# Kernel optimization log

Measured on AMD Instinct MI355X. Metric: run time of the kernel, lower is better.

Reference implementation:

```python
import jax, jax.numpy as jnp
import numpy as np
from jax import lax

N, C, L = 64, 64, 8192

def setup_inputs() -> dict:
    key = jax.random.key(0)
    k1, k2, k3 = jax.random.split(key, 3)
    observes = jax.random.normal(k1, (N, C, L), dtype=jnp.float32)
    transitions = jax.random.normal(k2, (C, C), dtype=jnp.float32) * 0.1
    target = jax.random.randint(k3, (N, L), 0, C, dtype=jnp.int64)
    return {"observes": observes, "transitions": transitions, "target": target}

def reference(observes, transitions, target):
    # Batched linear-chain CRF negative log-likelihood, averaged over batch.
    # observes: [N, C, L] emission scores; transitions: [C, C]; target: [N, L] int labels.
    em = jnp.transpose(observes, (0, 2, 1))  # [N, L, C]
    # Score of the gold path: emissions at gold labels + transitions between consecutive labels.
    gold_em = jnp.take_along_axis(em, target[..., None], axis=2)[..., 0].sum(axis=1)  # [N]
    gold_tr = transitions[target[:, :-1], target[:, 1:]].sum(axis=1)                  # [N]
    gold_score = gold_em + gold_tr
    # Forward algorithm (log-sum-exp DP over sequence length), batched over N.
    def step(alpha, e_t):
        # alpha: [N, C] log-scores ending in each state; e_t: [N, C]
        new_alpha = jax.nn.logsumexp(alpha[:, :, None] + transitions[None, :, :], axis=1) + e_t
        return new_alpha, None
    alpha0 = em[:, 0]                                  # [N, C]
    rest = jnp.moveaxis(em[:, 1:], 1, 0)               # [L-1, N, C] for scan
    alpha_T, _ = lax.scan(step, alpha0, rest)
    log_Z = jax.nn.logsumexp(alpha_T, axis=1)          # [N]
    nll = log_Z - gold_score                           # per-sample CRF loss
    return nll.sum() / nll.shape[0]
```

## Files before the change

### kernel.cpp

```cpp
#include <hip/hip_runtime.h>

#define NB 64
#define CS 64
#define LL 8192

#ifndef __has_builtin
#define __has_builtin(x) 0
#endif

__device__ __forceinline__ float uif(unsigned int u) { return __uint_as_float(u); }
__device__ __forceinline__ unsigned int fiu(float f) { return __float_as_uint(f); }

#define FMAC_DPP(ACC, Q, EV, R)                                                 \
  asm volatile("v_fmac_f32_dpp %0, %1, %2 row_ror:" #R                          \
               " row_mask:0xf bank_mask:0xf"                                    \
               : "+v"(ACC) : "v"(Q), "v"(EV))

#define ROW4(R)                                                                 \
  FMAC_DPP(acc0, qr0, Em[0][R], R);                                             \
  FMAC_DPP(acc1, qr1, Em[1][R], R);                                             \
  FMAC_DPP(acc2, qr2, Em[2][R], R);                                             \
  FMAC_DPP(acc3, qr3, Em[3][R], R)

__global__ __launch_bounds__(64, 1)
void crf_scan(const float* __restrict__ obs, const float* __restrict__ trans,
              float* __restrict__ out) {
  const int n = blockIdx.x;
  const int j = threadIdx.x;

  int w = __builtin_amdgcn_update_dpp(0, j, 0x121 , 0xf, 0xf, true);
  const int dsel = __builtin_amdgcn_readlane(w, 1);

  float Em[4][16];
#pragma unroll
  for (int g = 0; g < 4; ++g) {
#pragma unroll
    for (int r = 0; r < 16; ++r) {
      int irm = (j - r) & 15;
      int irp = (j + r) & 15;
      int ir = (dsel == 0) ? irm : irp;
      Em[g][r] = __expf(trans[(16 * g + ir) * CS + j]);
    }
  }

  const float* __restrict__ row = obs + ((size_t)n * CS + j) * (size_t)LL;
  float4 a0 = *(const float4*)(row);
  float4 a1 = *(const float4*)(row + 4);

  float q = __expf(a0.x);
  int carry = 0;

#pragma unroll 1
  for (int c = 0; c < LL / 8; ++c) {
    const int cn = (c + 1 < LL / 8) ? c + 1 : (LL / 8 - 1);
    float4 b0 = *(const float4*)(row + 8 * cn);
    float4 b1 = *(const float4*)(row + 8 * cn + 4);

    float ee[8];
    ee[0] = __expf(a0.x); ee[1] = __expf(a0.y);
    ee[2] = __expf(a0.z); ee[3] = __expf(a0.w);
    ee[4] = __expf(a1.x); ee[5] = __expf(a1.y);
    ee[6] = __expf(a1.z); ee[7] = __expf(a1.w);

#pragma unroll
    for (int k = 0; k < 8; ++k) {
      if (c == 0 && k == 0) continue;

#if __has_builtin(__builtin_amdgcn_permlane16_swap) && \
    __has_builtin(__builtin_amdgcn_permlane32_swap)
      unsigned qb = fiu(q);
      auto h = __builtin_amdgcn_permlane16_swap(qb, qb, false, false);
      auto A = __builtin_amdgcn_permlane32_swap(h[0], h[0], false, false);
      auto B = __builtin_amdgcn_permlane32_swap(h[1], h[1], false, false);
      float qr0 = uif(A[0]), qr2 = uif(A[1]);
      float qr1 = uif(B[0]), qr3 = uif(B[1]);
#else
      float qr0 = __shfl(q,  0 + (j & 15), 64);
      float qr1 = __shfl(q, 16 + (j & 15), 64);
      float qr2 = __shfl(q, 32 + (j & 15), 64);
      float qr3 = __shfl(q, 48 + (j & 15), 64);
#endif

      float acc0 = qr0 * Em[0][0];
      float acc1 = qr1 * Em[1][0];
      float acc2 = qr2 * Em[2][0];
      float acc3 = qr3 * Em[3][0];
      asm volatile("s_nop 1" :::);
      ROW4(1);  ROW4(2);  ROW4(3);  ROW4(4);  ROW4(5);
      ROW4(6);  ROW4(7);  ROW4(8);  ROW4(9);  ROW4(10);
      ROW4(11); ROW4(12); ROW4(13); ROW4(14); ROW4(15);
      float s = (acc0 + acc1) + (acc2 + acc3);
      q = s * ee[k];

      if ((k & 3) == 3) {
        unsigned q0 = (unsigned)__builtin_amdgcn_readfirstlane((int)fiu(q));
        int e = (int)((q0 >> 23) & 0xffu) - 126;
        q = ldexpf(q, -e);
        carry += e;
      }
    }
    a0 = b0; a1 = b1;
  }

  float s = q;
#pragma unroll
  for (int off = 32; off > 0; off >>= 1) s += __shfl_xor(s, off, 64);
  if (j == 0) {
    float logZ = (float)carry * 0.6931471805599453f + __logf(s);
    atomicAdd(out, logZ * (1.0f / NB));
  }
}

__global__ __launch_bounds__(256)
void crf_gold(const float* __restrict__ obs, const float* __restrict__ trans,
              const int* __restrict__ tgt, float* __restrict__ out) {
  const int n = blockIdx.x;
  const int tid = threadIdx.x;
  const int* __restrict__ trow = tgt + (size_t)n * LL;
  float acc = 0.f;
  for (int t = tid; t < LL; t += 256) {
    int s = trow[t];
    acc += obs[((size_t)n * CS + s) * (size_t)LL + t];
    if (t + 1 < LL) acc += trans[s * CS + trow[t + 1]];
  }
#pragma unroll
  for (int off = 32; off > 0; off >>= 1) acc += __shfl_xor(acc, off, 64);
  __shared__ float red[4];
  if ((tid & 63) == 0) red[tid >> 6] = acc;
  __syncthreads();
  if (tid == 0) {
    float tot = red[0] + red[1] + red[2] + red[3];
    atomicAdd(out, -tot * (1.0f / NB));
  }
}

extern "C" void kernel_launch(void* const* d_in, const int* in_sizes, int n_in,
                              void* d_out, int out_size, void* d_ws, size_t ws_size,
                              hipStream_t stream) {
  const float* obs   = (const float*)d_in[0];
  const float* trans = (const float*)d_in[1];
  const int*   tgt   = (const int*)d_in[2];
  float* out = (float*)d_out;

  hipMemsetAsync(out, 0, sizeof(float), stream);
  crf_gold<<<NB, 256, 0, stream>>>(obs, trans, tgt, out);
  crf_scan<<<NB, 64, 0, stream>>>(obs, trans, out);
}
```

Measured before the change: 1.664 ms.

## Fuse gold-score and forward-scan kernels into one launch

Merges the gold-path kernel and the forward-scan kernel into a single launch of 2*NB blocks. The first NB blocks run the scan on one wavefront and the rest compute the gold score, so both run concurrently instead of back to back. It also replaces ldexpf renormalisation with a direct exponent-bit subtraction, and turns the transition and emission arrays into named scalars so they stay in registers. Each scan block now reserves 256 threads while only 64 do work, and the bit-subtraction renormalisation does not handle denormal or zero values.

```diff
diff --git a/kernel.cpp b/kernel.cpp
--- a/kernel.cpp
+++ b/kernel.cpp
@@ -4,44 +4,48 @@
 #define CS 64
 #define LL 8192
 
-#ifndef __has_builtin
-#define __has_builtin(x) 0
-#endif
-
 __device__ __forceinline__ float uif(unsigned int u) { return __uint_as_float(u); }
 __device__ __forceinline__ unsigned int fiu(float f) { return __float_as_uint(f); }
 
-#define FMAC_DPP(ACC, Q, EV, R)                                                 \
+#define E_(G, R) Em_##G##_##R
+
+#define DECL_E16(G)                                                             \
+  float E_(G, 0), E_(G, 1), E_(G, 2), E_(G, 3), E_(G, 4), E_(G, 5), E_(G, 6),   \
+      E_(G, 7), E_(G, 8), E_(G, 9), E_(G, 10), E_(G, 11), E_(G, 12),            \
+      E_(G, 13), E_(G, 14), E_(G, 15)
+
+#define INIT_E(G, R)                                                            \
+  E_(G, R) = __expf(trans[(16 * G +                                             \
+                           ((dsel == 0) ? ((j - R) & 15) : ((j + R) & 15))) *   \
+                              CS +                                              \
+                          j])
+
+#define INIT_E16(G)                                                             \
+  INIT_E(G, 0);  INIT_E(G, 1);  INIT_E(G, 2);  INIT_E(G, 3);                    \
+  INIT_E(G, 4);  INIT_E(G, 5);  INIT_E(G, 6);  INIT_E(G, 7);                    \
+  INIT_E(G, 8);  INIT_E(G, 9);  INIT_E(G, 10); INIT_E(G, 11);                   \
+  INIT_E(G, 12); INIT_E(G, 13); INIT_E(G, 14); INIT_E(G, 15)
+
+#define FMAC_DPP(ACC, Q, G, R)                                                  \
   asm volatile("v_fmac_f32_dpp %0, %1, %2 row_ror:" #R                          \
                " row_mask:0xf bank_mask:0xf"                                    \
-               : "+v"(ACC) : "v"(Q), "v"(EV))
+               : "+v"(ACC) : "v"(Q), "v"(E_(G, R)))
 
 #define ROW4(R)                                                                 \
-  FMAC_DPP(acc0, qr0, Em[0][R], R);                                             \
-  FMAC_DPP(acc1, qr1, Em[1][R], R);                                             \
-  FMAC_DPP(acc2, qr2, Em[2][R], R);                                             \
-  FMAC_DPP(acc3, qr3, Em[3][R], R)
+  FMAC_DPP(acc0, qr0, 0, R);                                                    \
+  FMAC_DPP(acc1, qr1, 1, R);                                                    \
+  FMAC_DPP(acc2, qr2, 2, R);                                                    \
+  FMAC_DPP(acc3, qr3, 3, R)
 
-__global__ __launch_bounds__(64, 1)
-void crf_scan(const float* __restrict__ obs, const float* __restrict__ trans,
-              float* __restrict__ out) {
-  const int n = blockIdx.x;
-  const int j = threadIdx.x;
-
+__device__ __forceinline__ void crf_scan_block(const float* __restrict__ obs,
+                                               const float* __restrict__ trans,
+                                               float* __restrict__ out,
+                                               int n, int j) {
   int w = __builtin_amdgcn_update_dpp(0, j, 0x121 , 0xf, 0xf, true);
   const int dsel = __builtin_amdgcn_readlane(w, 1);
 
-  float Em[4][16];
-#pragma unroll
-  for (int g = 0; g < 4; ++g) {
-#pragma unroll
-    for (int r = 0; r < 16; ++r) {
-      int irm = (j - r) & 15;
-      int irp = (j + r) & 15;
-      int ir = (dsel == 0) ? irm : irp;
-      Em[g][r] = __expf(trans[(16 * g + ir) * CS + j]);
-    }
-  }
+  DECL_E16(0); DECL_E16(1); DECL_E16(2); DECL_E16(3);
+  INIT_E16(0); INIT_E16(1); INIT_E16(2); INIT_E16(3);
 
   const float* __restrict__ row = obs + ((size_t)n * CS + j) * (size_t)LL;
   float4 a0 = *(const float4*)(row);
@@ -56,47 +60,39 @@
     float4 b0 = *(const float4*)(row + 8 * cn);
     float4 b1 = *(const float4*)(row + 8 * cn + 4);
 
-    float ee[8];
-    ee[0] = __expf(a0.x); ee[1] = __expf(a0.y);
-    ee[2] = __expf(a0.z); ee[3] = __expf(a0.w);
-    ee[4] = __expf(a1.x); ee[5] = __expf(a1.y);
-    ee[6] = __expf(a1.z); ee[7] = __expf(a1.w);
+    float e0 = __expf(a0.x), e1 = __expf(a0.y), e2 = __expf(a0.z),
+          e3 = __expf(a0.w), e4 = __expf(a1.x), e5 = __expf(a1.y),
+          e6 = __expf(a1.z), e7 = __expf(a1.w);
 
 #pragma unroll
     for (int k = 0; k < 8; ++k) {
       if (c == 0 && k == 0) continue;
 
-#if __has_builtin(__builtin_amdgcn_permlane16_swap) && \
-    __has_builtin(__builtin_amdgcn_permlane32_swap)
       unsigned qb = fiu(q);
       auto h = __builtin_amdgcn_permlane16_swap(qb, qb, false, false);
       auto A = __builtin_amdgcn_permlane32_swap(h[0], h[0], false, false);
       auto B = __builtin_amdgcn_permlane32_swap(h[1], h[1], false, false);
       float qr0 = uif(A[0]), qr2 = uif(A[1]);
       float qr1 = uif(B[0]), qr3 = uif(B[1]);
-#else
-      float qr0 = __shfl(q,  0 + (j & 15), 64);
-      float qr1 = __shfl(q, 16 + (j & 15), 64);
-      float qr2 = __shfl(q, 32 + (j & 15), 64);
-      float qr3 = __shfl(q, 48 + (j & 15), 64);
-#endif
 
-      float acc0 = qr0 * Em[0][0];
-      float acc1 = qr1 * Em[1][0];
-      float acc2 = qr2 * Em[2][0];
-      float acc3 = qr3 * Em[3][0];
+      float acc0 = qr0 * E_(0, 0);
+      float acc1 = qr1 * E_(1, 0);
+      float acc2 = qr2 * E_(2, 0);
+      float acc3 = qr3 * E_(3, 0);
       asm volatile("s_nop 1" :::);
       ROW4(1);  ROW4(2);  ROW4(3);  ROW4(4);  ROW4(5);
       ROW4(6);  ROW4(7);  ROW4(8);  ROW4(9);  ROW4(10);
       ROW4(11); ROW4(12); ROW4(13); ROW4(14); ROW4(15);
       float s = (acc0 + acc1) + (acc2 + acc3);
-      q = s * ee[k];
+      float ee = (k == 0) ? e0 : (k == 1) ? e1 : (k == 2) ? e2 : (k == 3) ? e3
+               : (k == 4) ? e4 : (k == 5) ? e5 : (k == 6) ? e6 : e7;
+      q = s * ee;
 
       if ((k & 3) == 3) {
-        unsigned q0 = (unsigned)__builtin_amdgcn_readfirstlane((int)fiu(q));
-        int e = (int)((q0 >> 23) & 0xffu) - 126;
-        q = ldexpf(q, -e);
+        int q0 = __builtin_amdgcn_readfirstlane((int)fiu(q));
+        int e = ((q0 >> 23) & 0xff) - 126;
         carry += e;
+        q = uif(fiu(q) - (unsigned)(e << 23));
       }
     }
     a0 = b0; a1 = b1;
@@ -111,10 +107,10 @@
   }
 }
 
-__global__ __launch_bounds__(256)
-void crf_gold(const float* __restrict__ obs, const float* __restrict__ trans,
-              const int* __restrict__ tgt, float* __restrict__ out) {
-  const int n = blockIdx.x;
+__device__ __forceinline__ void crf_gold_block(const float* __restrict__ obs,
+                                               const float* __restrict__ trans,
+                                               const int* __restrict__ tgt,
+                                               float* __restrict__ out, int n) {
   const int tid = threadIdx.x;
   const int* __restrict__ trow = tgt + (size_t)n * LL;
   float acc = 0.f;
@@ -134,6 +130,18 @@
   }
 }
 
+__global__ __launch_bounds__(256, 1)
+void crf_fused(const float* __restrict__ obs, const float* __restrict__ trans,
+               const int* __restrict__ tgt, float* __restrict__ out) {
+  const int b = blockIdx.x;
+  if (b < NB) {
+    if (threadIdx.x < 64)
+      crf_scan_block(obs, trans, out, b, threadIdx.x);
+  } else {
+    crf_gold_block(obs, trans, tgt, out, b - NB);
+  }
+}
+
 extern "C" void kernel_launch(void* const* d_in, const int* in_sizes, int n_in,
                               void* d_out, int out_size, void* d_ws, size_t ws_size,
                               hipStream_t stream) {
@@ -143,6 +151,5 @@
   float* out = (float*)d_out;
 
   hipMemsetAsync(out, 0, sizeof(float), stream);
-  crf_gold<<<NB, 256, 0, stream>>>(obs, trans, tgt, out);
-  crf_scan<<<NB, 64, 0, stream>>>(obs, trans, out);
+  crf_fused<<<2 * NB, 256, 0, stream>>>(obs, trans, tgt, out);
 }
```

After: 1.603 ms. 1.04x faster.
